# Kernel optimization log

Hardware: AMD Instinct MI355X
Metric: run time of the kernel (lower is better)

Reference implementation:

```python
import jax, jax.numpy as jnp
import numpy as np

N, E, IN_DIM, H, C = 100000, 1600000, 128, 4, 64
NEG_SLOPE = 0.2
BN_EPS = 1e-5


def setup_inputs() -> dict:
    key = jax.random.key(0)
    ks = jax.random.split(key, 9)
    s = 1.0 / np.sqrt(IN_DIM)
    return {
        "feature": jax.random.normal(ks[0], (N, IN_DIM), dtype=jnp.float32),
        "edge_index": jax.random.randint(ks[1], (2, E), 0, N, dtype=jnp.int64),
        "W_l": jax.random.uniform(ks[2], (IN_DIM, H * C), jnp.float32, -s, s),
        "b_l": jnp.zeros((H * C,), jnp.float32),
        "W_r": jax.random.uniform(ks[3], (IN_DIM, H * C), jnp.float32, -s, s),
        "b_r": jnp.zeros((H * C,), jnp.float32),
        "att": jax.random.normal(ks[4], (H, C), dtype=jnp.float32) * 0.1,
        "bias": jnp.zeros((H * C,), jnp.float32),
        "gamma": jnp.ones((H * C,), jnp.float32),
        "beta": jnp.zeros((H * C,), jnp.float32),
    }


def reference(feature, edge_index, W_l, b_l, W_r, b_r, att, bias, gamma, beta):
    n = feature.shape[0]
    # add self loops (add_self_loops=True)
    loops = jnp.arange(n, dtype=edge_index.dtype)
    src = jnp.concatenate([edge_index[0], loops])
    dst = jnp.concatenate([edge_index[1], loops])
    # GATv2: separate source/target linear projections -> [N, H, C]
    x_l = (feature @ W_l + b_l).reshape(n, H, C)
    x_r = (feature @ W_r + b_r).reshape(n, H, C)
    # per-edge attention score: a^T LeakyReLU(x_l[src] + x_r[dst])  [Etot, H]
    e = jax.nn.leaky_relu(x_l[src] + x_r[dst], NEG_SLOPE)
    alpha = jnp.einsum('ehc,hc->eh', e, att)
    # segment softmax over incoming edges per target node
    amax = jax.ops.segment_max(alpha, dst, num_segments=n)  # [N, H]
    alpha = jnp.exp(alpha - amax[dst])
    denom = jax.ops.segment_sum(alpha, dst, num_segments=n)  # [N, H]
    alpha = alpha / (denom[dst] + 1e-16)
    # weighted scatter-aggregate of source messages
    out = jax.ops.segment_sum(x_l[src] * alpha[:, :, None], dst, num_segments=n)
    out = out.reshape(n, H * C) + bias  # concat=True
    # BatchNorm1d (training: batch statistics over nodes)
    mean = out.mean(axis=0)
    var = out.var(axis=0)
    out = (out - mean) / jnp.sqrt(var + BN_EPS) * gamma + beta
    return jax.nn.relu(out)
```

## Files before the change

### kernel.cpp

```cpp
#include <hip/hip_runtime.h>
#include <cstdint>

#define IN_DIM 128
#define HC 256
#define NEG_SLOPE 0.2f
#define BN_EPS 1e-5f
#define LOG2E 1.44269504088896340736f

#define BKT_SHIFT 9
#define BKT_CAP 16384
#define B_SC 512
#define NB_BN 1024

typedef short bf16x8 __attribute__((ext_vector_type(8)));
typedef float f32x4 __attribute__((ext_vector_type(4)));

#define EXP2F(x) __builtin_amdgcn_exp2f(x)

__device__ __forceinline__ unsigned short f2bf(float f) {
    union { float f; unsigned int u; } v; v.f = f;
    unsigned int r = (v.u + 0x7FFFu + ((v.u >> 16) & 1u)) >> 16;
    return (unsigned short)r;
}
__device__ __forceinline__ float bf2f(unsigned short h) {
    union { unsigned int u; float f; } v; v.u = ((unsigned int)h) << 16;
    return v.f;
}

template<int CTRL>
__device__ __forceinline__ float dppadd(float x) {
    int y = __builtin_amdgcn_update_dpp(0, __builtin_bit_cast(int, x), CTRL, 0xF, 0xF, true);
    return x + __builtin_bit_cast(float, y);
}
__device__ __forceinline__ float red16(float p) {
    p = dppadd<0xB1>(p);
    p = dppadd<0x4E>(p);
    p = dppadd<0x124>(p);
    p = dppadd<0x128>(p);
    return p;
}

__device__ __forceinline__ void unpk(ushort4 u, float* f) {
    f[0] = bf2f(u.x); f[1] = bf2f(u.y); f[2] = bf2f(u.z); f[3] = bf2f(u.w);
}
__device__ __forceinline__ float esc(const float* f, float x0, float x1, float x2, float x3,
                                     float4 a) {
    float z0 = f[0] + x0, z1 = f[1] + x1, z2 = f[2] + x2, z3 = f[3] + x3;
    float p = a.x * fmaxf(z0, NEG_SLOPE * z0);
    p = fmaf(a.y, fmaxf(z1, NEG_SLOPE * z1), p);
    p = fmaf(a.z, fmaxf(z2, NEG_SLOPE * z2), p);
    p = fmaf(a.w, fmaxf(z3, NEG_SLOPE * z3), p);
    return p;
}

__global__ __launch_bounds__(256) void prep(
    const float* __restrict__ Wl, const float* __restrict__ Wr,
    unsigned short* __restrict__ Wfrag, int* __restrict__ gcur)
{
    int b = blockIdx.x;
    if (b < 32) {
        int ob = b * 4 + (threadIdx.x >> 6);
        int j = ob >> 2;
        int kk = ob & 3;
        int l = threadIdx.x & 63;
        int col = j * 16 + (l & 15);
        const float* W = (col < 256) ? Wl : Wr;
        int c = col & 255;
        unsigned short tmp[8];
#pragma unroll
        for (int m = 0; m < 8; ++m) {
            int k = kk * 32 + ((l >> 4) << 3) + m;
            tmp[m] = f2bf(W[(size_t)k * 256 + c]);
        }
        ulonglong2* dst = (ulonglong2*)(Wfrag + ((size_t)(j * 4 + kk) * 64 + l) * 8);
        *dst = *(ulonglong2*)tmp;
    } else {
        gcur[threadIdx.x] = 0;
    }
}

__global__ __launch_bounds__(256) void scatter_gemm(
    const float* __restrict__ F, const unsigned short* __restrict__ Wfrag,
    const float* __restrict__ bl, const float* __restrict__ br,
    unsigned short* __restrict__ xl, unsigned short* __restrict__ xr,
    const int* __restrict__ ei, int* __restrict__ gcur, int2* __restrict__ bucketBuf,
    int E, int n, int ntiles)
{
    int b = blockIdx.x;
    if (b < B_SC) {
        __shared__ int hist[256];
        __shared__ int base[256];
        int t = threadIdx.x;
        hist[t] = 0;
        __syncthreads();
        int ept = (E + B_SC - 1) / B_SC;
        int beg = b * ept;
        int endc = min(beg + ept, E);
        for (int e = beg + t; e < endc; e += 256) {
            int dst = ei[(size_t)E + e];
            atomicAdd(&hist[dst >> BKT_SHIFT], 1);
        }
        __syncthreads();
        int h = hist[t];
        if (h > 0) base[t] = atomicAdd(&gcur[t], h);
        hist[t] = 0;
        __syncthreads();
        for (int e = beg + t; e < endc; e += 256) {
            int src = ei[e];
            int dst = ei[(size_t)E + e];
            int bk = dst >> BKT_SHIFT;
            int r = atomicAdd(&hist[bk], 1);
            int pos = base[bk] + r;
            if (pos < BKT_CAP) {
                int2 v; v.x = src; v.y = dst;
                bucketBuf[(size_t)bk * BKT_CAP + pos] = v;
            }
        }
        return;
    }
    int i = (b - B_SC) * 4 + (threadIdx.x >> 6);
    if (i >= ntiles) return;
    int l = threadIdx.x & 63;

    int row = i * 16 + (l & 15);
    bf16x8 afr[4];
#pragma unroll
    for (int kk = 0; kk < 4; ++kk) {
        int k0 = kk * 32 + ((l >> 4) << 3);
        float4 f0 = make_float4(0.f, 0.f, 0.f, 0.f), f1 = f0;
        if (row < n) {
            const float* p = F + (size_t)row * IN_DIM + k0;
            f0 = *(const float4*)p;
            f1 = *(const float4*)(p + 4);
        }
        unsigned short tmp[8];
        tmp[0] = f2bf(f0.x); tmp[1] = f2bf(f0.y); tmp[2] = f2bf(f0.z); tmp[3] = f2bf(f0.w);
        tmp[4] = f2bf(f1.x); tmp[5] = f2bf(f1.y); tmp[6] = f2bf(f1.z); tmp[7] = f2bf(f1.w);
        afr[kk] = *(bf16x8*)tmp;
    }

    const bf16x8* wv = (const bf16x8*)Wfrag + l;
    int cl = l & 15;
    int rbase = i * 16 + ((l >> 4) << 2);

#pragma unroll 4
    for (int j = 0; j < 32; ++j) {
        const bf16x8* bp = wv + (size_t)j * 4 * 64;
        f32x4 acc = {0.f, 0.f, 0.f, 0.f};
        acc = __builtin_amdgcn_mfma_f32_16x16x32_bf16(afr[0], bp[0 * 64], acc, 0, 0, 0);
        acc = __builtin_amdgcn_mfma_f32_16x16x32_bf16(afr[1], bp[1 * 64], acc, 0, 0, 0);
        acc = __builtin_amdgcn_mfma_f32_16x16x32_bf16(afr[2], bp[2 * 64], acc, 0, 0, 0);
        acc = __builtin_amdgcn_mfma_f32_16x16x32_bf16(afr[3], bp[3 * 64], acc, 0, 0, 0);

        int col = j * 16 + cl;
        unsigned short* X = (col < 256) ? xl : xr;
        int c = col & 255;
        float bv = (col < 256) ? bl[c] : br[c];
#pragma unroll
        for (int q = 0; q < 4; ++q) {
            int r = rbase + q;
            if (r < n) X[(size_t)r * HC + c] = f2bf(acc[q] + bv);
        }
    }
}

__global__ __launch_bounds__(256) void bucket_build(
    const int2* __restrict__ bucketBuf, const int* __restrict__ gcur,
    int* __restrict__ off, int* __restrict__ csr_boff, int n, int nbkt)
{
    __shared__ int bin[512];
    __shared__ int tmp[256];
    __shared__ int bstart_sh;
    int b = blockIdx.x;
    int t = threadIdx.x;

    int part = (t < b) ? min(gcur[t], BKT_CAP) : 0;
    tmp[t] = part;
    __syncthreads();
    for (int d = 128; d > 0; d >>= 1) {
        if (t < d) tmp[t] += tmp[t + d];
        __syncthreads();
    }
    if (t == 0) bstart_sh = tmp[0];
    __syncthreads();
    int bstart = bstart_sh;
    int cnt_b = min(gcur[b], BKT_CAP);

    bin[t] = 0; bin[t + 256] = 0;
    __syncthreads();

    const int2* buf = bucketBuf + (size_t)b * BKT_CAP;
    int nodeBase = b << BKT_SHIFT;

    for (int i = t; i < cnt_b; i += 256) {
        atomicAdd(&bin[buf[i].y - nodeBase], 1);
    }
    __syncthreads();

    int b0 = bin[2 * t], b1 = bin[2 * t + 1];
    tmp[t] = b0 + b1;
    __syncthreads();
    for (int d = 1; d < 256; d <<= 1) {
        int v = (t >= d) ? tmp[t - d] : 0;
        __syncthreads();
        tmp[t] += v;
        __syncthreads();
    }
    int excl = (t == 0) ? 0 : tmp[t - 1];
    int lo0 = excl, lo1 = excl + b0;

    int n0 = nodeBase + 2 * t, n1 = n0 + 1;
    if (n0 < n) off[n0] = bstart + lo0;
    if (n1 < n) off[n1] = bstart + lo1;
    int nodeEnd = min(nodeBase + 512, n);
    if (t == 0 && nodeEnd == n) off[n] = bstart + cnt_b;

    bin[2 * t] = lo0; bin[2 * t + 1] = lo1;
    __syncthreads();
    for (int i = t; i < cnt_b; i += 256) {
        int2 e = buf[i];
        int r = atomicAdd(&bin[e.y - nodeBase], 1);
        csr_boff[bstart + r] = e.x << 9;
    }
}

__global__ __launch_bounds__(256) void gat_agg(
    const unsigned short* __restrict__ xl, const unsigned short* __restrict__ xr,
    const int* __restrict__ csr_boff, const int* __restrict__ off,
    const float* __restrict__ att, const float* __restrict__ bias,
    unsigned short* __restrict__ outb, int n)
{
    int d = (blockIdx.x * blockDim.x + threadIdx.x) >> 6;
    int lane = threadIdx.x & 63;
    if (d >= n) return;

    const char* xlc = (const char*)xl;
    int lo8 = lane << 3;
    ushort4 xru = ((const ushort4*)xr)[(size_t)d * 64 + lane];
    float xr0 = bf2f(xru.x), xr1 = bf2f(xru.y), xr2 = bf2f(xru.z), xr3 = bf2f(xru.w);
    float4 att4 = *(const float4*)(att + 4 * lane);
    att4.x *= LOG2E; att4.y *= LOG2E; att4.z *= LOG2E; att4.w *= LOG2E;

    int beg = __builtin_amdgcn_readfirstlane(off[d]);
    int end = __builtin_amdgcn_readfirstlane(off[d + 1]);

    float ax, ay, az, aw, lsum;
    {
        ushort4 t0 = *(const ushort4*)(xlc + ((size_t)d << 9) + lo8);
        float f0[4];
        unpk(t0, f0);
        float p0 = esc(f0, xr0, xr1, xr2, xr3, att4);
        p0 = red16(p0);
        float e0 = EXP2F(p0);
        ax = e0 * f0[0]; ay = e0 * f0[1]; az = e0 * f0[2]; aw = e0 * f0[3];
        lsum = e0;
    }

    int nmain = (end - beg) & ~3;
    int imend = beg + nmain;
    int i = beg;

    ushort4 u0, u1, u2, u3;
    ushort4 v0, v1, v2, v3;
    if (i < imend) {
        int b0 = __builtin_amdgcn_readfirstlane(csr_boff[i]);
        int b1 = __builtin_amdgcn_readfirstlane(csr_boff[i + 1]);
        int b2 = __builtin_amdgcn_readfirstlane(csr_boff[i + 2]);
        int b3 = __builtin_amdgcn_readfirstlane(csr_boff[i + 3]);
        u0 = *(const ushort4*)(xlc + b0 + lo8);
        u1 = *(const ushort4*)(xlc + b1 + lo8);
        u2 = *(const ushort4*)(xlc + b2 + lo8);
        u3 = *(const ushort4*)(xlc + b3 + lo8);
    }
    if (i + 4 < imend) {
        int b0 = __builtin_amdgcn_readfirstlane(csr_boff[i + 4]);
        int b1 = __builtin_amdgcn_readfirstlane(csr_boff[i + 5]);
        int b2 = __builtin_amdgcn_readfirstlane(csr_boff[i + 6]);
        int b3 = __builtin_amdgcn_readfirstlane(csr_boff[i + 7]);
        v0 = *(const ushort4*)(xlc + b0 + lo8);
        v1 = *(const ushort4*)(xlc + b1 + lo8);
        v2 = *(const ushort4*)(xlc + b2 + lo8);
        v3 = *(const ushort4*)(xlc + b3 + lo8);
    }
    while (i < imend) {
        ushort4 c0 = u0, c1 = u1, c2 = u2, c3 = u3;
        u0 = v0; u1 = v1; u2 = v2; u3 = v3;
        int ipf = i + 8;
        if (ipf < imend) {
            int b0 = __builtin_amdgcn_readfirstlane(csr_boff[ipf]);
            int b1 = __builtin_amdgcn_readfirstlane(csr_boff[ipf + 1]);
            int b2 = __builtin_amdgcn_readfirstlane(csr_boff[ipf + 2]);
            int b3 = __builtin_amdgcn_readfirstlane(csr_boff[ipf + 3]);
            v0 = *(const ushort4*)(xlc + b0 + lo8);
            v1 = *(const ushort4*)(xlc + b1 + lo8);
            v2 = *(const ushort4*)(xlc + b2 + lo8);
            v3 = *(const ushort4*)(xlc + b3 + lo8);
        }
        float f0[4], f1[4], f2[4], f3[4];
        unpk(c0, f0); unpk(c1, f1); unpk(c2, f2); unpk(c3, f3);

        float p0 = esc(f0, xr0, xr1, xr2, xr3, att4);
        float p1 = esc(f1, xr0, xr1, xr2, xr3, att4);
        float p2 = esc(f2, xr0, xr1, xr2, xr3, att4);
        float p3 = esc(f3, xr0, xr1, xr2, xr3, att4);

        p0 = dppadd<0xB1>(p0);  p1 = dppadd<0xB1>(p1);  p2 = dppadd<0xB1>(p2);  p3 = dppadd<0xB1>(p3);
        p0 = dppadd<0x4E>(p0);  p1 = dppadd<0x4E>(p1);  p2 = dppadd<0x4E>(p2);  p3 = dppadd<0x4E>(p3);
        p0 = dppadd<0x124>(p0); p1 = dppadd<0x124>(p1); p2 = dppadd<0x124>(p2); p3 = dppadd<0x124>(p3);
        p0 = dppadd<0x128>(p0); p1 = dppadd<0x128>(p1); p2 = dppadd<0x128>(p2); p3 = dppadd<0x128>(p3);

        float e0 = EXP2F(p0), e1 = EXP2F(p1);
        float e2 = EXP2F(p2), e3 = EXP2F(p3);
        ax = fmaf(e0, f0[0], fmaf(e1, f1[0], fmaf(e2, f2[0], fmaf(e3, f3[0], ax))));
        ay = fmaf(e0, f0[1], fmaf(e1, f1[1], fmaf(e2, f2[1], fmaf(e3, f3[1], ay))));
        az = fmaf(e0, f0[2], fmaf(e1, f1[2], fmaf(e2, f2[2], fmaf(e3, f3[2], az))));
        aw = fmaf(e0, f0[3], fmaf(e1, f1[3], fmaf(e2, f2[3], fmaf(e3, f3[3], aw))));
        lsum += (e0 + e1) + (e2 + e3);
        i += 4;
    }
    for (; i < end; ++i) {
        int b0 = __builtin_amdgcn_readfirstlane(csr_boff[i]);
        ushort4 t0 = *(const ushort4*)(xlc + b0 + lo8);
        float f0[4];
        unpk(t0, f0);
        float p0 = esc(f0, xr0, xr1, xr2, xr3, att4);
        p0 = red16(p0);
        float e0 = EXP2F(p0);
        ax = fmaf(e0, f0[0], ax); ay = fmaf(e0, f0[1], ay);
        az = fmaf(e0, f0[2], az); aw = fmaf(e0, f0[3], aw);
        lsum += e0;
    }

    float inv = 1.f / (lsum + 1e-16f);
    float4 b4 = *(const float4*)(bias + 4 * lane);
    ushort4 o;
    o.x = f2bf(fmaf(ax, inv, b4.x));
    o.y = f2bf(fmaf(ay, inv, b4.y));
    o.z = f2bf(fmaf(az, inv, b4.z));
    o.w = f2bf(fmaf(aw, inv, b4.w));
    ((ushort4*)outb)[(size_t)d * 64 + lane] = o;
}

__global__ __launch_bounds__(256) void bn_partial(const unsigned short* __restrict__ outb,
                                                  float* __restrict__ partials, int n)
{
    int c = threadIdx.x;
    int b = blockIdx.x;
    int chunk = (n + NB_BN - 1) / NB_BN;
    int beg = b * chunk;
    int end = min(beg + chunk, n);
    float s = 0.f, s2 = 0.f;
    for (int r = beg; r < end; ++r) {
        float v = bf2f(outb[(size_t)r * HC + c]);
        s += v; s2 += v * v;
    }
    partials[(size_t)b * 512 + c] = s;
    partials[(size_t)b * 512 + 256 + c] = s2;
}

__global__ __launch_bounds__(256) void bn_final(const float* __restrict__ partials,
                                                float* __restrict__ stats, int n)
{
    int c = blockIdx.x;
    int t = threadIdx.x;
    float s = 0.f, s2 = 0.f;
    for (int b = t; b < NB_BN; b += 256) {
        s  += partials[(size_t)b * 512 + c];
        s2 += partials[(size_t)b * 512 + 256 + c];
    }
    __shared__ float rs[256], rs2[256];
    rs[t] = s; rs2[t] = s2;
    __syncthreads();
    for (int d = 128; d > 0; d >>= 1) {
        if (t < d) { rs[t] += rs[t + d]; rs2[t] += rs2[t + d]; }
        __syncthreads();
    }
    if (t == 0) {
        float mean = rs[0] / (float)n;
        float var = rs2[0] / (float)n - mean * mean;
        stats[c] = mean;
        stats[256 + c] = rsqrtf(var + BN_EPS);
    }
}

__global__ void bn_apply(const unsigned short* __restrict__ outb,
                         const float* __restrict__ stats,
                         const float* __restrict__ gamma, const float* __restrict__ beta,
                         float* __restrict__ out, long long total4)
{
    long long stride = (long long)gridDim.x * blockDim.x;
    for (long long i = blockIdx.x * (long long)blockDim.x + threadIdx.x; i < total4;
         i += stride) {
        int cb = ((int)(i & 63)) * 4;
        ushort4 u = ((const ushort4*)outb)[i];
        float4 o;
        o.x = fmaxf(0.f, (bf2f(u.x) - stats[cb + 0]) * stats[256 + cb + 0] * gamma[cb + 0] + beta[cb + 0]);
        o.y = fmaxf(0.f, (bf2f(u.y) - stats[cb + 1]) * stats[256 + cb + 1] * gamma[cb + 1] + beta[cb + 1]);
        o.z = fmaxf(0.f, (bf2f(u.z) - stats[cb + 2]) * stats[256 + cb + 2] * gamma[cb + 2] + beta[cb + 2]);
        o.w = fmaxf(0.f, (bf2f(u.w) - stats[cb + 3]) * stats[256 + cb + 3] * gamma[cb + 3] + beta[cb + 3]);
        ((float4*)out)[i] = o;
    }
}

extern "C" void kernel_launch(void* const* d_in, const int* in_sizes, int n_in,
                              void* d_out, int out_size, void* d_ws, size_t ws_size,
                              hipStream_t stream)
{
    const float* feature = (const float*)d_in[0];
    const int* ei        = (const int*)d_in[1];
    const float* Wl   = (const float*)d_in[2];
    const float* bl   = (const float*)d_in[3];
    const float* Wr   = (const float*)d_in[4];
    const float* br   = (const float*)d_in[5];
    const float* att  = (const float*)d_in[6];
    const float* bias = (const float*)d_in[7];
    const float* gamma = (const float*)d_in[8];
    const float* beta  = (const float*)d_in[9];

    const int n = in_sizes[0] / IN_DIM;
    const int E = in_sizes[1] / 2;
    const int ntiles = (n + 15) / 16;
    const int nbkt = (n + 511) >> 9;

    char* ws = (char*)d_ws;
    size_t o = 0;
    auto carve = [&](size_t bytes) -> void* {
        void* p = ws + o; o = (o + bytes + 15) & ~(size_t)15; return p;
    };
    unsigned short* xl    = (unsigned short*)carve((size_t)n * HC * sizeof(short));
    unsigned short* xr    = (unsigned short*)carve((size_t)n * HC * sizeof(short));
    unsigned short* outb  = (unsigned short*)carve((size_t)n * HC * sizeof(short));
    unsigned short* Wfrag = (unsigned short*)carve((size_t)32 * 4 * 64 * 8 * sizeof(short));
    int2* bucketBuf = (int2*)carve((size_t)256 * BKT_CAP * sizeof(int2));
    int*  csr_boff  = (int*)carve((size_t)E * sizeof(int));
    int*  off       = (int*)carve((size_t)(n + 1) * sizeof(int));
    int*  gcur      = (int*)carve(256 * sizeof(int));
    float* partials = (float*)carve((size_t)NB_BN * 512 * sizeof(float));
    float* stats    = (float*)carve(512 * sizeof(float));
    float* outf = (float*)d_out;

    if (o > ws_size) return;

    prep<<<33, 256, 0, stream>>>(Wl, Wr, Wfrag, gcur);

    scatter_gemm<<<B_SC + (ntiles + 3) / 4, 256, 0, stream>>>(
        feature, Wfrag, bl, br, xl, xr, ei, gcur, bucketBuf, E, n, ntiles);

    bucket_build<<<nbkt, 256, 0, stream>>>(bucketBuf, gcur, off, csr_boff, n, nbkt);

    int agg_blocks = (n + 3) / 4;
    gat_agg<<<agg_blocks, 256, 0, stream>>>(xl, xr, csr_boff, off, att, bias, outb, n);

    bn_partial<<<NB_BN, 256, 0, stream>>>(outb, partials, n);
    bn_final<<<256, 256, 0, stream>>>(partials, stats, n);
    long long total4 = (long long)n * (HC / 4);
    bn_apply<<<4096, 256, 0, stream>>>(outb, stats, gamma, beta, outf, total4);
}
```

Measured before the change: 322.8 us.

## Stage edge chunks in LDS and locally sort by bucket before global scatter

The bucketing phase now loads each block's edge chunk into shared memory once, builds a histogram, prefix-scans it, and counting-sorts the edges locally by destination bucket. It then writes them to the global bucket buffer so consecutive threads write contiguous positions within a bucket. This is meant to remove the second global read of edge_index and make the scattered global writes more coalesced. The block count rises from 512 to 768 so each chunk fits in a fixed LDS buffer. The cost is about 37KB of LDS per block, which lowers occupancy, plus extra barriers for the scan. If the per-block chunk exceeds CHUNK_MAX the block silently does nothing.

Result: no change. 316.6 us (-1.9%).

```diff
diff --git a/kernel.cpp b/kernel.cpp
--- a/kernel.cpp
+++ b/kernel.cpp
@@ -9,7 +9,8 @@
 
 #define BKT_SHIFT 9
 #define BKT_CAP 16384
-#define B_SC 512
+#define B_SC 768
+#define CHUNK_MAX 2304
 #define NB_BN 1024
 
 typedef short bf16x8 __attribute__((ext_vector_type(8)));
@@ -88,33 +89,55 @@
 {
     int b = blockIdx.x;
     if (b < B_SC) {
+        __shared__ int2 eL[CHUNK_MAX];
+        __shared__ int2 sortedL[CHUNK_MAX];
         __shared__ int hist[256];
+        __shared__ int lofs[256];
         __shared__ int base[256];
         int t = threadIdx.x;
-        hist[t] = 0;
-        __syncthreads();
         int ept = (E + B_SC - 1) / B_SC;
         int beg = b * ept;
-        int endc = min(beg + ept, E);
-        for (int e = beg + t; e < endc; e += 256) {
-            int dst = ei[(size_t)E + e];
-            atomicAdd(&hist[dst >> BKT_SHIFT], 1);
-        }
+        int cnt = E - beg;
+        if (cnt > ept) cnt = ept;
+        if (cnt < 0) cnt = 0;
+        if (ept > CHUNK_MAX) return;
+
+        for (int k = t; k < cnt; k += 256) {
+            int2 v;
+            v.x = ei[beg + k];
+            v.y = ei[(size_t)E + beg + k];
+            eL[k] = v;
+        }
+        hist[t] = 0;
+        __syncthreads();
+        for (int k = t; k < cnt; k += 256) atomicAdd(&hist[eL[k].y >> BKT_SHIFT], 1);
         __syncthreads();
         int h = hist[t];
+        lofs[t] = h;
+        __syncthreads();
+        for (int dl = 1; dl < 256; dl <<= 1) {
+            int v = (t >= dl) ? lofs[t - dl] : 0;
+            __syncthreads();
+            lofs[t] += v;
+            __syncthreads();
+        }
+        int excl = lofs[t] - h;
         if (h > 0) base[t] = atomicAdd(&gcur[t], h);
-        hist[t] = 0;
-        __syncthreads();
-        for (int e = beg + t; e < endc; e += 256) {
-            int src = ei[e];
-            int dst = ei[(size_t)E + e];
-            int bk = dst >> BKT_SHIFT;
-            int r = atomicAdd(&hist[bk], 1);
-            int pos = base[bk] + r;
-            if (pos < BKT_CAP) {
-                int2 v; v.x = src; v.y = dst;
-                bucketBuf[(size_t)bk * BKT_CAP + pos] = v;
-            }
+        hist[t] = excl;
+        __syncthreads();
+        lofs[t] = excl;
+        __syncthreads();
+        for (int k = t; k < cnt; k += 256) {
+            int2 e = eL[k];
+            int r = atomicAdd(&hist[e.y >> BKT_SHIFT], 1);
+            sortedL[r] = e;
+        }
+        __syncthreads();
+        for (int k = t; k < cnt; k += 256) {
+            int2 e = sortedL[k];
+            int bk = e.y >> BKT_SHIFT;
+            int pos = base[bk] + (k - lofs[bk]);
+            if (pos < BKT_CAP) bucketBuf[(size_t)bk * BKT_CAP + pos] = e;
         }
         return;
     }
```
